# Kernel optimization log

Hardware: AMD Instinct MI355X
Metric: run time of the kernel (lower is better)

## Reference

```python
import jax, jax.numpy as jnp
import numpy as np

B = 1      # batch
D = 64     # octree grid side at this level
N = 65536  # active voxels
C = 32     # channels (nin == nout for resblock)
K = 3      # kernel size


def _offsets():
    r = jnp.arange(K) - K // 2
    oz, oy, ox = jnp.meshgrid(r, r, r, indexing='ij')
    return jnp.stack([oz.ravel(), oy.ravel(), ox.ravel()], axis=-1)  # [27,3] (kz,ky,kx order)


def octree_conv3d(values, indices, mask_values, kernel, bias, activation=None):
    # values: [N,Cin], indices: [N,4] (b,z,y,x), mask_values: [N,1]
    Cin = values.shape[-1]
    Cout = kernel.shape[-1]
    taps = kernel.reshape(K * K * K, Cin, Cout)            # kz,ky,kx order == kernel[kz,ky,kx]
    vals = jnp.einsum('nc,tcd->tnd', values, taps)         # [27,N,Cout]
    offs = _offsets()                                      # [27,3]
    coords = indices[:, 1:]                                # [N,3]
    # shift = [0, kz-1, ky-1, kx-1]; clamp to [0, D-1] (stride=inv_stride=1)
    sh = jnp.clip(coords[None, :, :] + offs[:, None, :], 0, D - 1)  # [27,N,3]
    lin = indices[:, 0][None, :] * (D * D * D) + sh[..., 0] * (D * D) + sh[..., 1] * D + sh[..., 2]
    grid = jnp.zeros((B * D * D * D, Cout), dtype=values.dtype)
    grid = grid.at[lin.reshape(-1)].add(vals.reshape(-1, Cout))     # scatter-add == coalesce sum
    out_lin = indices[:, 0] * (D * D * D) + coords[:, 0] * (D * D) + coords[:, 1] * D + coords[:, 2]
    gathered = grid[out_lin]                               # [N,Cout] values at mask positions
    out = (gathered + mask_values * bias[None, :]) * mask_values     # result + mask*bias; result*mask
    if activation is not None:
        out = activation(out)
    return out


def setup_inputs() -> dict:
    key = jax.random.key(0)
    k1, k2, k3, k4, k5, k6 = jax.random.split(key, 6)
    G = B * D * D * D
    perm = jax.random.permutation(k1, G)[:N]               # unique (coalesced) voxel indices
    b = perm // (D * D * D)
    rem = perm % (D * D * D)
    z = rem // (D * D)
    y = (rem // D) % D
    x = rem % D
    indices = jnp.stack([b, z, y, x], axis=-1).astype(jnp.int64)   # [N,4]
    values = jax.random.normal(k2, (N, C), dtype=jnp.float32)
    mask_values = jnp.ones((N, 1), dtype=jnp.float32)
    stdv = 1.0 / np.sqrt(K * K * K * C)
    kern1 = (jax.random.uniform(k3, (K, K, K, C, C)) - 0.5) * 2.0 * stdv
    bias1 = (jax.random.uniform(k4, (C,)) - 0.5) * 2.0 * stdv
    kern2 = (jax.random.uniform(k5, (K, K, K, C, C)) - 0.5) * 2.0 * stdv
    bias2 = (jax.random.uniform(k6, (C,)) - 0.5) * 2.0 * stdv
    return {'values': values, 'indices': indices, 'mask_values': mask_values,
            'kern1': kern1, 'bias1': bias1, 'kern2': kern2, 'bias2': bias2}


def reference(values, indices, mask_values, kern1, bias1, kern2, bias2):
    # OctreeResblock: conv(relu) -> conv -> residual add, all on the sparse index set
    h = octree_conv3d(values, indices, mask_values, kern1, bias1, activation=jax.nn.relu)
    h = octree_conv3d(h, indices, mask_values, kern2, bias2, activation=None)
    return values + h
```

## Files before the change

### kernel.cpp

```cpp
#include <hip/hip_runtime.h>

#define NPTS 65536
#define CCH  32
#define DDIM 64
#define GVOX (DDIM*DDIM*DDIM)
#define MAXTILES 4128

typedef _Float16 half8  __attribute__((ext_vector_type(8)));
typedef _Float16 half4v __attribute__((ext_vector_type(4)));
typedef float    floatx4 __attribute__((ext_vector_type(4)));

__global__ __launch_bounds__(256) void k_prep0(
    int* __restrict__ map, int* __restrict__ sorted,
    const float* __restrict__ values, _Float16* __restrict__ valsh,
    const float* __restrict__ k1, const float* __restrict__ k2,
    _Float16* __restrict__ w1, _Float16* __restrict__ w2,
    _Float16* __restrict__ hh, int* __restrict__ pcoord,
    int* __restrict__ cnt, int* __restrict__ slot)
{
  int tid = blockIdx.x * 256 + threadIdx.x;
  if (tid < GVOX/4) { ((int4*)map)[tid] = make_int4(-1,-1,-1,-1); return; }
  tid -= GVOX/4;
  if (tid < MAXTILES*16) { sorted[tid] = NPTS; return; }
  tid -= MAXTILES*16;
  if (tid < (NPTS*CCH)/4) {
    float4 v = ((const float4*)values)[tid];
    half4v h = { (_Float16)v.x, (_Float16)v.y, (_Float16)v.z, (_Float16)v.w };
    ((half4v*)valsh)[tid] = h; return;
  }
  tid -= (NPTS*CCH)/4;
  if (tid < 27*CCH*CCH) {
    int t = tid/(CCH*CCH), r = tid%(CCH*CCH);
    int cin = r/CCH, cout = r%CCH;
    int o = (t*CCH + cout)*CCH + cin;
    w1[o] = (_Float16)k1[tid]; w2[o] = (_Float16)k2[tid]; return;
  }
  tid -= 27*CCH*CCH;
  if (tid < CCH) { valsh[NPTS*CCH+tid] = (_Float16)0.f; hh[NPTS*CCH+tid] = (_Float16)0.f; return; }
  tid -= CCH;
  if (tid < 27) { cnt[tid] = 0; slot[tid] = 0; return; }
  tid -= 27;
  if (tid == 0) pcoord[NPTS] = 0;
}
#define PREP0_THREADS (GVOX/4 + MAXTILES*16 + (NPTS*CCH)/4 + 27*CCH*CCH + CCH + 27 + 1)

__global__ __launch_bounds__(256) void k_prep1(const int* __restrict__ idx,
                                               int* __restrict__ map,
                                               int* __restrict__ pcoord,
                                               int* __restrict__ cls,
                                               int* __restrict__ cnt)
{
  __shared__ int lcnt[27];
  if (threadIdx.x < 27) lcnt[threadIdx.x] = 0;
  __syncthreads();
  const int n = blockIdx.x*256 + threadIdx.x;
  const int4 v = ((const int4*)idx)[n];
  const int b = v.x, z = v.y, y = v.z, x = v.w;
  map[((b*DDIM + z)*DDIM + y)*DDIM + x] = n;
  pcoord[n] = (b<<18) | (z<<12) | (y<<6) | x;
  const int cz = (z==0)?0:((z==DDIM-1)?2:1);
  const int cy = (y==0)?0:((y==DDIM-1)?2:1);
  const int cx = (x==0)?0:((x==DDIM-1)?2:1);
  const int c = cz*9 + cy*3 + cx;
  cls[n] = c;
  atomicAdd(&lcnt[c], 1);
  __syncthreads();
  if (threadIdx.x < 27 && lcnt[threadIdx.x]) atomicAdd(&cnt[threadIdx.x], lcnt[threadIdx.x]);
}

__global__ __launch_bounds__(256) void k_prep3(const int* __restrict__ cls,
                                               const int* __restrict__ cnt,
                                               int* __restrict__ slot,
                                               int* __restrict__ sorted,
                                               int* __restrict__ tileclass,
                                               int* __restrict__ ntiles)
{
  __shared__ int s_clsbase[27];
  __shared__ int s_tstart[28];
  if (threadIdx.x == 0) {
    int b = 0, tb = 0;
#pragma unroll
    for (int c = 0; c < 27; ++c) {
      s_clsbase[c] = b; s_tstart[c] = tb;
      const int ntc = (cnt[c] + 15) >> 4;
      b += ntc << 4; tb += ntc;
    }
    s_tstart[27] = tb;
    if (blockIdx.x == 0) *ntiles = tb;
  }
  __syncthreads();

  if (blockIdx.x < NPTS/256) {
    __shared__ int lcnt[27], lbase[27];
    if (threadIdx.x < 27) lcnt[threadIdx.x] = 0;
    __syncthreads();
    const int n = blockIdx.x*256 + threadIdx.x;
    const int c = cls[n];
    const int lrank = atomicAdd(&lcnt[c], 1);
    __syncthreads();
    if (threadIdx.x < 27)
      lbase[threadIdx.x] = lcnt[threadIdx.x] ? atomicAdd(&slot[threadIdx.x], lcnt[threadIdx.x]) : 0;
    __syncthreads();
    sorted[s_clsbase[c] + lbase[c] + lrank] = n;
  } else {
    const int i = (blockIdx.x - NPTS/256)*256 + threadIdx.x;
    if (i >= MAXTILES) return;
    const int nt = s_tstart[27];
    int c = 13;
    if (i < nt) {
      for (int cc = 0; cc < 27; ++cc)
        if (i >= s_tstart[cc] && i < s_tstart[cc+1]) { c = cc; break; }
    }
    tileclass[i] = c;
  }
}

template<int J0, int J1>
__device__ __forceinline__ void accum_taps(
    const _Float16* __restrict__ A, const int* __restrict__ map,
    const _Float16* lw,
    int cz, int cy, int cx, int linb,
    const int* az, const int* ay, const int* ax,
    int m, int quad, floatx4& acc0, floatx4& acc1)
{
  int srcs[J1 - J0];
#pragma unroll
  for (int j = J0; j < J1; ++j) {
    const int jz = j/9, jy = (j/3)%3, jx = j%3;
    const int s = map[linb | az[jz] | ay[jy] | ax[jx]];
    srcs[j - J0] = (s < 0) ? (NPTS*CCH) : (s*CCH);
  }
#pragma unroll
  for (int j = J0; j < J1; ++j) {
    const int jz = j/9, jy = (j/3)%3, jx = j%3;
    const int tz = (cz==1) ? (2-jz) : ((jz==1) ? 1 : ((cz==0) ? 0 : 2));
    const int ty = (cy==1) ? (2-jy) : ((jy==1) ? 1 : ((cy==0) ? 0 : 2));
    const int tx = (cx==1) ? (2-jx) : ((jx==1) ? 1 : ((cx==0) ? 0 : 2));
    const int t  = tz*9 + ty*3 + tx;
    half8 a  = *(const half8*)(A + srcs[j - J0] + quad*8);
    const _Float16* wr = lw + t*(CCH*CCH);
    half8 b0 = *(const half8*)(wr + m*CCH + quad*8);
    half8 b1 = *(const half8*)(wr + (16+m)*CCH + quad*8);
    acc0 = __builtin_amdgcn_mfma_f32_16x16x32_f16(a, b0, acc0, 0, 0, 0);
    acc1 = __builtin_amdgcn_mfma_f32_16x16x32_f16(a, b1, acc1, 0, 0, 0);
  }
}

template<int MODE>
__global__ __launch_bounds__(512) void conv_mfma(
    const _Float16* __restrict__ A,
    const int* __restrict__ map,
    const int* __restrict__ pcoord,
    const int* __restrict__ sorted,
    const int* __restrict__ tileclass,
    const int* __restrict__ ntp,
    const _Float16* __restrict__ WT,
    const float* __restrict__ bias,
    const float* __restrict__ mask,
    const float* __restrict__ resid,
    _Float16* __restrict__ hout,
    float* __restrict__ fout)
{
  __shared__ _Float16 lw[27*CCH*CCH];
  __shared__ float red[4][16][33];

  for (int i = threadIdx.x; i < 3456; i += 512)
    ((half8*)lw)[i] = ((const half8*)WT)[i];

  const int wv   = threadIdx.x >> 6;
  const int tl   = wv >> 1;
  const int half = wv & 1;
  const int tile = blockIdx.x*4 + tl;
  const int nt   = *ntp;
  const bool active = tile < nt;
  const int lane = threadIdx.x & 63;
  const int m = lane & 15, quad = lane >> 4;

  floatx4 acc0 = {0.f,0.f,0.f,0.f};
  floatx4 acc1 = {0.f,0.f,0.f,0.f};

  int scls = 13, pc = 0;
  if (active) {
    scls = __builtin_amdgcn_readfirstlane(tileclass[tile]);
    const int pid = sorted[tile*16 + m];
    pc = pcoord[pid];
  }
  __syncthreads();

  if (active) {
    const int cz = scls/9, cy = (scls/3)%3, cx = scls%3;
    const int bb = pc>>18, z = (pc>>12)&63, y = (pc>>6)&63, x = pc&63;
    const int linb = bb << 18;
    const int az[3] = { max(z-1,0)<<12, z<<12, min(z+1,DDIM-1)<<12 };
    const int ay[3] = { max(y-1,0)<<6,  y<<6,  min(y+1,DDIM-1)<<6 };
    const int ax[3] = { max(x-1,0),     x,     min(x+1,DDIM-1) };
    if (half == 0)
      accum_taps<0,14>(A, map, lw, cz,cy,cx, linb, az,ay,ax, m,quad, acc0,acc1);
    else
      accum_taps<14,27>(A, map, lw, cz,cy,cx, linb, az,ay,ax, m,quad, acc0,acc1);
  }

  if (active && half == 0) {
#pragma unroll
    for (int r = 0; r < 4; ++r) {
      red[tl][quad*4+r][m]    = acc0[r];
      red[tl][quad*4+r][m+16] = acc1[r];
    }
  }
  __syncthreads();
  if (active && half == 1) {
#pragma unroll
    for (int r = 0; r < 4; ++r) {
      acc0[r] += red[tl][quad*4+r][m];
      acc1[r] += red[tl][quad*4+r][m+16];
    }
    const float bi0 = bias[m], bi1 = bias[m+16];
#pragma unroll
    for (int reg = 0; reg < 4; ++reg) {
      const int r  = quad*4 + reg;
      const int pr = sorted[tile*16 + r];
      if (pr >= NPTS) continue;
      const float mk = mask[pr];
      float v0 = (acc0[reg] + mk*bi0) * mk;
      float v1 = (acc1[reg] + mk*bi1) * mk;
      if (MODE == 0) {
        v0 = fmaxf(v0, 0.f); v1 = fmaxf(v1, 0.f);
        hout[pr*CCH + m]      = (_Float16)v0;
        hout[pr*CCH + m + 16] = (_Float16)v1;
      } else {
        fout[pr*CCH + m]      = resid[pr*CCH + m]      + v0;
        fout[pr*CCH + m + 16] = resid[pr*CCH + m + 16] + v1;
      }
    }
  }
}


extern "C" void kernel_launch(void* const* d_in, const int* in_sizes, int n_in,
                              void* d_out, int out_size, void* d_ws, size_t ws_size,
                              hipStream_t stream) {
  const float* values = (const float*)d_in[0];
  const int*   indices= (const int*)  d_in[1];
  const float* maskv  = (const float*)d_in[2];
  const float* kern1  = (const float*)d_in[3];
  const float* bias1  = (const float*)d_in[4];
  const float* kern2  = (const float*)d_in[5];
  const float* bias2  = (const float*)d_in[6];
  float* out = (float*)d_out;

  char* ws = (char*)d_ws;
  size_t off = 0;
  auto alloc = [&](size_t bytes) { void* p = ws + off; off = (off + bytes + 255) & ~(size_t)255; return p; };
  int*      map      = (int*)     alloc(GVOX*4);
  int*      pcoord   = (int*)     alloc((NPTS+1)*4);
  int*      cls      = (int*)     alloc(NPTS*4);
  int*      sorted   = (int*)     alloc(MAXTILES*16*4);
  int*      tileclass= (int*)     alloc(MAXTILES*4);
  int*      cnt      = (int*)     alloc(27*4);
  int*      slot     = (int*)     alloc(27*4);
  int*      ntiles   = (int*)     alloc(4);
  _Float16* valsh    = (_Float16*)alloc((NPTS+1)*CCH*2);
  _Float16* hh       = (_Float16*)alloc((NPTS+1)*CCH*2);
  _Float16* wt1      = (_Float16*)alloc(27*CCH*CCH*2);
  _Float16* wt2      = (_Float16*)alloc(27*CCH*CCH*2);

  k_prep0<<<(PREP0_THREADS + 255)/256, 256, 0, stream>>>(
      map, sorted, values, valsh, kern1, kern2, wt1, wt2, hh, pcoord, cnt, slot);
  k_prep1<<<NPTS/256, 256, 0, stream>>>(indices, map, pcoord, cls, cnt);
  k_prep3<<<NPTS/256 + (MAXTILES+255)/256, 256, 0, stream>>>(
      cls, cnt, slot, sorted, tileclass, ntiles);

  conv_mfma<0><<<MAXTILES/4, 512, 0, stream>>>(valsh, map, pcoord, sorted, tileclass,
                                               ntiles, wt1, bias1, maskv, nullptr, hh, nullptr);
  conv_mfma<1><<<MAXTILES/4, 512, 0, stream>>>(hh, map, pcoord, sorted, tileclass,
                                               ntiles, wt2, bias2, maskv, values, nullptr, out);
}
```

Measured before the change: 141.1 us.

## Fuse all prep and conv stages into one cooperative persistent kernel

Replaces the five separate launches (init, map build, class sort, two convolutions) with one cooperative kernel of 256 blocks x 1024 threads that separates the phases with grid-wide syncs. Each block computes the per-class tile starts itself and loops over tiles persistently, with the weights staged in shared memory. This removes the launch gaps and per-launch tail effects, and keeps the old multi-kernel path as a fallback. In exchange it adds grid-sync overhead and limits the conv phase to 256 resident blocks.

New measurement: 140.4 us. About the same (-0.5%).

```diff
diff --git a/kernel.cpp b/kernel.cpp
--- a/kernel.cpp
+++ b/kernel.cpp
@@ -1,14 +1,196 @@
 #include <hip/hip_runtime.h>
+#include <hip/hip_cooperative_groups.h>
+
+namespace cg = cooperative_groups;
 
 #define NPTS 65536
 #define CCH  32
 #define DDIM 64
 #define GVOX (DDIM*DDIM*DDIM)
 #define MAXTILES 4128
+#define NTHREADS 1024
+#define NBLOCKS  256
+#define TTOT (NTHREADS*NBLOCKS)
 
 typedef _Float16 half8  __attribute__((ext_vector_type(8)));
 typedef _Float16 half4v __attribute__((ext_vector_type(4)));
 typedef float    floatx4 __attribute__((ext_vector_type(4)));
+
+#define P0N (GVOX/4 + MAXTILES*16 + (NPTS*CCH)/4 + 27*CCH*CCH + CCH + 27 + 1)
+
+struct SharedC {
+  _Float16 lw[27*CCH*CCH];
+  int tstart[28];
+  int clsbase[27];
+  int lcnt[27];
+  int lbase[27];
+};
+
+template<int MODE>
+__device__ void conv_phase_c(SharedC& sh,
+    const _Float16* __restrict__ A, const int* __restrict__ map,
+    const int* __restrict__ pcoord, const int* __restrict__ sorted,
+    const _Float16* __restrict__ WT, const float* __restrict__ bias,
+    const float* __restrict__ mask, const float* __restrict__ resid,
+    _Float16* __restrict__ hout, float* __restrict__ fout)
+{
+  for (int i = threadIdx.x; i < (27*CCH*CCH)/8; i += NTHREADS)
+    ((half8*)sh.lw)[i] = ((const half8*)WT)[i];
+  __syncthreads();
+
+  const int wv   = threadIdx.x >> 6;
+  const int lane = threadIdx.x & 63;
+  const int m = lane & 15, quad = lane >> 4;
+  const int nt = sh.tstart[27];
+  const float bi0 = bias[m], bi1 = bias[m+16];
+
+  for (int tile = blockIdx.x*(NTHREADS/64) + wv; tile < nt;
+       tile += NBLOCKS*(NTHREADS/64)) {
+    int scls = 0;
+    for (int cc = 1; cc < 27; ++cc) if (tile >= sh.tstart[cc]) scls = cc;
+    scls = __builtin_amdgcn_readfirstlane(scls);
+    const int cz = scls/9, cy = (scls/3)%3, cx = scls%3;
+
+    const int pid = sorted[tile*16 + m];
+    const int pc  = pcoord[pid];
+    const int bb = pc>>18, z = (pc>>12)&63, y = (pc>>6)&63, x = pc&63;
+    const int linb = bb << 18;
+    const int az[3] = { max(z-1,0)<<12, z<<12, min(z+1,DDIM-1)<<12 };
+    const int ay[3] = { max(y-1,0)<<6,  y<<6,  min(y+1,DDIM-1)<<6 };
+    const int ax[3] = { max(x-1,0),     x,     min(x+1,DDIM-1) };
+
+    floatx4 acc0 = {0.f,0.f,0.f,0.f};
+    floatx4 acc1 = {0.f,0.f,0.f,0.f};
+
+    int srcs[27];
+#pragma unroll
+    for (int j = 0; j < 27; ++j) {
+      const int jz = j/9, jy = (j/3)%3, jx = j%3;
+      const int s = map[linb | az[jz] | ay[jy] | ax[jx]];
+      srcs[j] = (s < 0) ? (NPTS*CCH) : (s*CCH);
+    }
+#pragma unroll
+    for (int j = 0; j < 27; ++j) {
+      const int jz = j/9, jy = (j/3)%3, jx = j%3;
+      const int tz = (cz==1) ? (2-jz) : ((jz==1) ? 1 : ((cz==0) ? 0 : 2));
+      const int ty = (cy==1) ? (2-jy) : ((jy==1) ? 1 : ((cy==0) ? 0 : 2));
+      const int tx = (cx==1) ? (2-jx) : ((jx==1) ? 1 : ((cx==0) ? 0 : 2));
+      const int t  = tz*9 + ty*3 + tx;
+      half8 a  = *(const half8*)(A + srcs[j] + quad*8);
+      const _Float16* wr = sh.lw + t*(CCH*CCH);
+      half8 b0 = *(const half8*)(wr + m*CCH + quad*8);
+      half8 b1 = *(const half8*)(wr + (16+m)*CCH + quad*8);
+      acc0 = __builtin_amdgcn_mfma_f32_16x16x32_f16(a, b0, acc0, 0, 0, 0);
+      acc1 = __builtin_amdgcn_mfma_f32_16x16x32_f16(a, b1, acc1, 0, 0, 0);
+    }
+
+#pragma unroll
+    for (int reg = 0; reg < 4; ++reg) {
+      const int r  = quad*4 + reg;
+      const int pr = sorted[tile*16 + r];
+      if (pr >= NPTS) continue;
+      const float mk = mask[pr];
+      float v0 = (acc0[reg] + mk*bi0) * mk;
+      float v1 = (acc1[reg] + mk*bi1) * mk;
+      if (MODE == 0) {
+        v0 = fmaxf(v0, 0.f); v1 = fmaxf(v1, 0.f);
+        hout[pr*CCH + m]      = (_Float16)v0;
+        hout[pr*CCH + m + 16] = (_Float16)v1;
+      } else {
+        fout[pr*CCH + m]      = resid[pr*CCH + m]      + v0;
+        fout[pr*CCH + m + 16] = resid[pr*CCH + m + 16] + v1;
+      }
+    }
+  }
+}
+
+__global__ __launch_bounds__(1024, 4) void mega2(
+    const float* __restrict__ values, const int* __restrict__ idx,
+    const float* __restrict__ maskv,
+    const float* __restrict__ k1, const float* __restrict__ bias1,
+    const float* __restrict__ k2, const float* __restrict__ bias2,
+    int* __restrict__ map, int* __restrict__ pcoord,
+    int* __restrict__ sorted, int* __restrict__ cnt, int* __restrict__ slot,
+    _Float16* __restrict__ valsh, _Float16* __restrict__ hh,
+    _Float16* __restrict__ wt1, _Float16* __restrict__ wt2,
+    float* __restrict__ out)
+{
+  __shared__ SharedC sh;
+  cg::grid_group grid = cg::this_grid();
+  const int gtid = blockIdx.x*NTHREADS + threadIdx.x;
+
+  for (int t0 = gtid; t0 < P0N; t0 += TTOT) {
+    int tid = t0;
+    if (tid < GVOX/4) { ((int4*)map)[tid] = make_int4(-1,-1,-1,-1); continue; }
+    tid -= GVOX/4;
+    if (tid < MAXTILES*16) { sorted[tid] = NPTS; continue; }
+    tid -= MAXTILES*16;
+    if (tid < (NPTS*CCH)/4) {
+      float4 v = ((const float4*)values)[tid];
+      half4v h = { (_Float16)v.x, (_Float16)v.y, (_Float16)v.z, (_Float16)v.w };
+      ((half4v*)valsh)[tid] = h; continue;
+    }
+    tid -= (NPTS*CCH)/4;
+    if (tid < 27*CCH*CCH) {
+      int t = tid/(CCH*CCH), r = tid%(CCH*CCH);
+      int cin = r/CCH, cout = r%CCH;
+      int o = (t*CCH + cout)*CCH + cin;
+      wt1[o] = (_Float16)k1[tid]; wt2[o] = (_Float16)k2[tid]; continue;
+    }
+    tid -= 27*CCH*CCH;
+    if (tid < CCH) { valsh[NPTS*CCH+tid] = (_Float16)0.f; hh[NPTS*CCH+tid] = (_Float16)0.f; continue; }
+    tid -= CCH;
+    if (tid < 27) { cnt[tid] = 0; slot[tid] = 0; continue; }
+    tid -= 27;
+    if (tid == 0) pcoord[NPTS] = 0;
+  }
+  grid.sync();
+
+  if (threadIdx.x < 27) sh.lcnt[threadIdx.x] = 0;
+  __syncthreads();
+  int myc = -1;
+  if (gtid < NPTS) {
+    const int4 v = ((const int4*)idx)[gtid];
+    const int b = v.x, z = v.y, y = v.z, x = v.w;
+    map[((b*DDIM + z)*DDIM + y)*DDIM + x] = gtid;
+    pcoord[gtid] = (b<<18) | (z<<12) | (y<<6) | x;
+    const int cz = (z==0)?0:((z==DDIM-1)?2:1);
+    const int cy = (y==0)?0:((y==DDIM-1)?2:1);
+    const int cx = (x==0)?0:((x==DDIM-1)?2:1);
+    myc = cz*9 + cy*3 + cx;
+    atomicAdd(&sh.lcnt[myc], 1);
+  }
+  __syncthreads();
+  if (threadIdx.x < 27 && sh.lcnt[threadIdx.x])
+    atomicAdd(&cnt[threadIdx.x], sh.lcnt[threadIdx.x]);
+  grid.sync();
+
+  if (threadIdx.x == 0) {
+    int b = 0, tb = 0;
+    for (int c = 0; c < 27; ++c) {
+      const int cv = atomicAdd(&cnt[c], 0);
+      sh.clsbase[c] = b; sh.tstart[c] = tb;
+      const int ntc = (cv + 15) >> 4;
+      b += ntc << 4; tb += ntc;
+    }
+    sh.tstart[27] = tb;
+  }
+  if (threadIdx.x < 27) sh.lcnt[threadIdx.x] = 0;
+  __syncthreads();
+  int lrank = 0;
+  if (gtid < NPTS) lrank = atomicAdd(&sh.lcnt[myc], 1);
+  __syncthreads();
+  if (threadIdx.x < 27)
+    sh.lbase[threadIdx.x] = sh.lcnt[threadIdx.x] ? atomicAdd(&slot[threadIdx.x], sh.lcnt[threadIdx.x]) : 0;
+  __syncthreads();
+  if (gtid < NPTS) sorted[sh.clsbase[myc] + sh.lbase[myc] + lrank] = gtid;
+  grid.sync();
+
+  conv_phase_c<0>(sh, valsh, map, pcoord, sorted, wt1, bias1, maskv, nullptr, hh, nullptr);
+  grid.sync();
+
+  conv_phase_c<1>(sh, hh, map, pcoord, sorted, wt2, bias2, maskv, values, nullptr, out);
+}
 
 __global__ __launch_bounds__(256) void k_prep0(
     int* __restrict__ map, int* __restrict__ sorted,
@@ -42,7 +224,6 @@
   tid -= 27;
   if (tid == 0) pcoord[NPTS] = 0;
 }
-#define PREP0_THREADS (GVOX/4 + MAXTILES*16 + (NPTS*CCH)/4 + 27*CCH*CCH + CCH + 27 + 1)
 
 __global__ __launch_bounds__(256) void k_prep1(const int* __restrict__ idx,
                                                int* __restrict__ map,
@@ -264,12 +445,33 @@
   _Float16* wt1      = (_Float16*)alloc(27*CCH*CCH*2);
   _Float16* wt2      = (_Float16*)alloc(27*CCH*CCH*2);
 
-  k_prep0<<<(PREP0_THREADS + 255)/256, 256, 0, stream>>>(
+  static int use_coop = -1;
+  if (use_coop < 0) {
+    int nb = 0;
+    hipError_t e = hipOccupancyMaxActiveBlocksPerMultiprocessor(
+        &nb, (const void*)mega2, NTHREADS, 0);
+    use_coop = (e == hipSuccess && nb >= 1) ? 1 : 0;
+  }
+
+  if (use_coop) {
+    void* args[] = { (void*)&values, (void*)&indices, (void*)&maskv,
+                     (void*)&kern1, (void*)&bias1, (void*)&kern2, (void*)&bias2,
+                     (void*)&map, (void*)&pcoord, (void*)&sorted,
+                     (void*)&cnt, (void*)&slot,
+                     (void*)&valsh, (void*)&hh, (void*)&wt1, (void*)&wt2,
+                     (void*)&out };
+    hipError_t e = hipLaunchCooperativeKernel((void*)mega2, dim3(NBLOCKS),
+                                              dim3(NTHREADS), args, 0, stream);
+    if (e == hipSuccess) return;
+    use_coop = 0;
+  }
+
+  k_prep0<<<((GVOX/4 + MAXTILES*16 + (NPTS*CCH)/4 + 27*CCH*CCH + CCH + 27 + 1) + 255)/256,
+            256, 0, stream>>>(
       map, sorted, values, valsh, kern1, kern2, wt1, wt2, hh, pcoord, cnt, slot);
   k_prep1<<<NPTS/256, 256, 0, stream>>>(indices, map, pcoord, cls, cnt);
   k_prep3<<<NPTS/256 + (MAXTILES+255)/256, 256, 0, stream>>>(
       cls, cnt, slot, sorted, tileclass, ntiles);
-
   conv_mfma<0><<<MAXTILES/4, 512, 0, stream>>>(valsh, map, pcoord, sorted, tileclass,
                                                ntiles, wt1, bias1, maskv, nullptr, hh, nullptr);
   conv_mfma<1><<<MAXTILES/4, 512, 0, stream>>>(hh, map, pcoord, sorted, tileclass,
```
